# Kernel tuning notes

Measured on AMD Instinct MI355X. Metric: run time of the kernel, lower is better.

Reference implementation:

```python
import jax, jax.numpy as jnp
import numpy as np
import math

# dims matching init_kwargs
B, N, CS, CZ = 1, 512, 384, 128
H, C, PQ, PV = 8, 128, 8, 8
INF, EPS = 1e5, 1e-8

# ---- quaternion / motor helpers (PGA motor encoded as [qw,qx,qy,qz,tx,ty,tz,0]) ----

def quat_conj(q):
    return q * jnp.array([1.0, -1.0, -1.0, -1.0], q.dtype)

def quat_mul(a, b):
    aw, ax, ay, az = jnp.split(a, 4, -1)
    bw, bx, by, bz = jnp.split(b, 4, -1)
    return jnp.concatenate([
        aw*bw - ax*bx - ay*by - az*bz,
        aw*bx + ax*bw + ay*bz - az*by,
        aw*by - ax*bz + ay*bw + az*bx,
        aw*bz + ax*by - ay*bx + az*bw], -1)

def quat_rotate(q, v):
    qv = q[..., 1:]
    uv = jnp.cross(qv, v)
    uuv = jnp.cross(qv, uv)
    return v + 2.0 * (q[..., :1] * uv + uuv)

def point_trafo(p, q, t):
    # p [...,K,3]; rigid transform by frame motor, homogeneous 4-vector out
    pp = quat_rotate(q, p) + t
    return jnp.concatenate([pp, jnp.ones_like(pp[..., :1])], -1)

def mv_transform(mv, q, t):
    # versor sandwich on a 16-dim multivector: three rotatable 3-vector blocks,
    # the point block (7:10, weight at 10) also translates; slots 0 and 10:16 invariant
    s0 = mv[..., 0:1]
    v1 = quat_rotate(q, mv[..., 1:4])
    v2 = quat_rotate(q, mv[..., 4:7])
    w = mv[..., 10:11]
    p = quat_rotate(q, mv[..., 7:10]) + w * t
    return jnp.concatenate([s0, v1, v2, p, mv[..., 10:16]], -1)

def mv_transform_inv(mv, q, t):
    qc = quat_conj(q)
    s0 = mv[..., 0:1]
    v1 = quat_rotate(qc, mv[..., 1:4])
    v2 = quat_rotate(qc, mv[..., 4:7])
    w = mv[..., 10:11]
    p = quat_rotate(qc, mv[..., 7:10] - w * t)
    return jnp.concatenate([s0, v1, v2, p, mv[..., 10:16]], -1)


def _forward(s, g, z, T, mask, W_q, b_q, W_kv, b_kv, W_qp, b_qp, W_kp, b_kp,
             W_vg, b_vg, W_mg, W_b, b_b, W_dz, b_dz, head_weights,
             softmax_weights, W_out, b_out, W_geo):
    T8 = T[..., :8]                                      # extract_motor
    qn = T8[..., :4]
    qn = qn / jnp.sqrt(jnp.sum(qn**2, -1, keepdims=True) + EPS)
    tr = T8[..., 4:7]

    q = (s @ W_q + b_q).reshape(B, N, H, C)
    kv = (s @ W_kv + b_kv).reshape(B, N, H, 2 * C)
    k, v = kv[..., :C], kv[..., C:]

    def make_pts(W, bb):
        # split into 3 chunks + stack(dim=-1) == reshape(...,3,HP).swapaxes
        p = (s @ W + bb).reshape(B, N, 3, H * PQ).swapaxes(-1, -2)  # [B,N,HP,3]
        p4 = point_trafo(p, qn[:, :, None, :], tr[:, :, None, :])
        return p4.reshape(B, N, H, PQ, 4)

    q_pts = make_pts(W_qp, b_qp)
    k_pts = make_pts(W_kp, b_kp)

    v_g = (s @ W_vg + b_vg).reshape(B, N, PV, 16)
    v_g = jnp.einsum('oi,bnic->bnoc', W_mg,
                     jnp.concatenate([v_g, g], -2)).reshape(B, N, H, PV, 16)

    bias = jnp.einsum('bijz,zh->bhij', z, W_b) + b_b[None, :, None, None]
    a = jnp.einsum('bihc,bjhc->bhij', q, k) * math.sqrt(1.0 / (3 * C))
    a = a + math.sqrt(1.0 / 3.0) * bias

    disp = q_pts[:, :, None, :, :, :3] - k_pts[:, None, :, :, :, :3]  # [B,N,N,H,P,3]
    pt = jnp.sum(disp**2, -1)                                         # [B,N,N,H,P]
    hw = jax.nn.softplus(head_weights) * math.sqrt(1.0 / (3 * (PQ * 9.0 / 2)))
    pt = -0.5 * jnp.sum(pt * hw[None, None, None, :, None], -1)       # [B,N,N,H]

    sq_mask = INF * (mask[:, :, None] * mask[:, None, :] - 1.0)
    a = a + pt.transpose(0, 3, 1, 2) + sq_mask[:, None]
    a = jax.nn.softmax(softmax_weights[None, :, None, None] * a, axis=-1)

    o = jnp.einsum('bhij,bjhc->bihc', a, v)                           # [B,N,H,C]

    qb, tb = qn[:, :, None, None, :], tr[:, :, None, None, :]
    vg_glob = mv_transform(v_g, qb, tb)
    o_g = jnp.einsum('bhij,bjhpc->bihpc', a, vg_glob)
    o_g = mv_transform_inv(o_g, qb, tb)                               # [B,N,H,PV,16]
    n1 = jnp.sqrt(jnp.sum(o_g[..., :10]**2, -1) + EPS)
    n2 = jnp.sqrt(jnp.sum(o_g[..., 10:]**2, -1) + EPS)
    o_g_norm = jnp.stack([n1, n2], -1)                                # [B,N,H,PV,2]

    # local relative frame features (8 per head)
    q_rel = quat_mul(quat_conj(qn)[:, :, None, :], qn[:, None, :, :])
    t_rel = quat_rotate(quat_conj(qn)[:, :, None, :], tr[:, None, :, :] - tr[:, :, None, :])
    rel = jnp.concatenate([q_rel, t_rel, jnp.zeros_like(t_rel[..., :1])], -1)  # [B,N,N,8]
    o_rel = jnp.einsum('bhij,bijc->bihc', a, rel)

    o_pair = jnp.einsum('bhij,bijc->bihc', a, z @ W_dz + b_dz)        # [B,N,H,CZ//4]

    feats = jnp.concatenate([o_pair, o, o_rel,
                             o_g.reshape(B, N, H, PV * 16),
                             o_g_norm.reshape(B, N, H, PV * 2)], -1).reshape(B, N, -1)
    s_out = feats @ W_out + b_out                                     # [B,N,CS]
    g_out = jnp.einsum('oi,bnic->bnoc', W_geo, o_g.reshape(B, N, H * PV, 16))
    return s_out, g_out


def setup_inputs() -> dict:
    key = jax.random.key(0)
    ks = jax.random.split(key, 32)
    def rn(i, shape, sc=1.0):
        return sc * jax.random.normal(ks[i], shape, jnp.float32)
    s = rn(0, (B, N, CS))
    g = rn(1, (B, N, PV, 16))
    z = rn(2, (B, N, N, CZ))
    Traw = rn(3, (B, N, 16))
    qn = Traw[..., :4]
    qn = qn / jnp.sqrt(jnp.sum(qn**2, -1, keepdims=True) + 1e-8)
    T = Traw.at[..., :4].set(qn).at[..., 4:7].multiply(3.0).at[..., 7:].set(0.0)
    mask = jnp.ones((B, N), jnp.float32)
    w = 0.02
    CAT = H * (CZ // 4 + C + 8 + PV * 18)   # 2496
    return dict(
        s=s, g=g, z=z, T=T, mask=mask,
        W_q=rn(4, (CS, H * C), w), b_q=jnp.zeros((H * C,), jnp.float32),
        W_kv=rn(5, (CS, 2 * H * C), w), b_kv=jnp.zeros((2 * H * C,), jnp.float32),
        W_qp=rn(6, (CS, H * PQ * 3), w), b_qp=jnp.zeros((H * PQ * 3,), jnp.float32),
        W_kp=rn(7, (CS, H * PQ * 3), w), b_kp=jnp.zeros((H * PQ * 3,), jnp.float32),
        W_vg=rn(8, (CS, PV * 16), w), b_vg=jnp.zeros((PV * 16,), jnp.float32),
        W_mg=rn(9, (H * PV, 2 * PV), 0.1),
        W_b=rn(10, (CZ, H), w), b_b=jnp.zeros((H,), jnp.float32),
        W_dz=rn(11, (CZ, CZ // 4), w), b_dz=jnp.zeros((CZ // 4,), jnp.float32),
        head_weights=-2.0 + 0.3 * rn(12, (H,)),
        softmax_weights=jnp.ones((H,), jnp.float32) + 0.1 * rn(13, (H,)),
        W_out=rn(14, (CAT, CS), w), b_out=jnp.zeros((CS,), jnp.float32),
        W_geo=rn(15, (PV, H * PV), 0.1))


def reference(s, g, z, T, mask, W_q, b_q, W_kv, b_kv, W_qp, b_qp, W_kp, b_kp,
              W_vg, b_vg, W_mg, W_b, b_b, W_dz, b_dz, head_weights,
              softmax_weights, W_out, b_out, W_geo):
    return _forward(s, g, z, T, mask, W_q, b_q, W_kv, b_kv, W_qp, b_qp, W_kp,
                    b_kp, W_vg, b_vg, W_mg, W_b, b_b, W_dz, b_dz, head_weights,
                    softmax_weights, W_out, b_out, W_geo)
```

## Files before the change

### kernel.cpp

```cpp
#include <hip/hip_runtime.h>
#include <math.h>

#define NN 512
#define CSD 384
#define CZD 128
#define HD 8
#define CD 128
#define EPSV 1e-8f
#define INFV 100000.0f

#define OFF_QN    ((size_t)0)
#define OFF_TR    ((size_t)2048)
#define OFF_ROWT  ((size_t)4096)
#define OFF_COLT  ((size_t)8192)
#define OFF_SB    ((size_t)12288)
#define OFF_QBUF  ((size_t)45056)
#define OFF_KV    ((size_t)569344)
#define OFF_QPR   ((size_t)1617920)
#define OFF_KPR   ((size_t)1716224)
#define OFF_VGR   ((size_t)1814528)
#define OFF_ZB    ((size_t)1880064)
#define OFF_A     ((size_t)3977216)
#define OFF_U     ((size_t)6074368)
#define OFF_V     ((size_t)6729728)
#define OFF_VP    ((size_t)7385088)
#define OFF_OB0   ((size_t)8433664)
#define OFF_OB1   ((size_t)8957952)
#define OFF_OG0   ((size_t)9482240)
#define OFF_OG1   ((size_t)10006528)
#define OFF_FEATS ((size_t)10530816)
#define OFF_PS    ((size_t)11808768)

__device__ __forceinline__ void qrot(const float q[4], const float* v, float* out) {
    float qw = q[0], qx = q[1], qy = q[2], qz = q[3];
    float ux = qy*v[2] - qz*v[1];
    float uy = qz*v[0] - qx*v[2];
    float uz = qx*v[1] - qy*v[0];
    float uux = qy*uz - qz*uy;
    float uuy = qz*ux - qx*uz;
    float uuz = qx*uy - qy*ux;
    out[0] = v[0] + 2.0f*(qw*ux + uux);
    out[1] = v[1] + 2.0f*(qw*uy + uuy);
    out[2] = v[2] + 2.0f*(qw*uz + uuz);
}

__device__ __forceinline__ void gemm_tiles(const float* __restrict__ A, int lda,
                                           const float* __restrict__ B, int ldb,
                                           int m0, int n0, int k0, int nk,
                                           float acc[4][4], float* AsT, float* Bs) {
    int t = threadIdx.x;
    int tx = t & 15, ty = t >> 4;
    int arow = t >> 3, ak4 = (t & 7) << 2;
    int brow = t >> 4, bc4 = (t & 15) << 2;
    const float* Ap0 = A + (size_t)(m0 + arow)*lda + ak4;
    const float* Ap1 = A + (size_t)(m0 + arow + 32)*lda + ak4;
    const float* Bp0 = B + (size_t)brow*ldb + n0 + bc4;
    const float* Bp1 = B + (size_t)(brow + 16)*ldb + n0 + bc4;
    float4 a0 = *(const float4*)(Ap0 + k0);
    float4 a1 = *(const float4*)(Ap1 + k0);
    float4 b0 = *(const float4*)(Bp0 + (size_t)k0*ldb);
    float4 b1 = *(const float4*)(Bp1 + (size_t)k0*ldb);
    for (int kc = 0; kc < nk; kc++) {
        AsT[(ak4+0)*68 + arow] = a0.x;
        AsT[(ak4+1)*68 + arow] = a0.y;
        AsT[(ak4+2)*68 + arow] = a0.z;
        AsT[(ak4+3)*68 + arow] = a0.w;
        AsT[(ak4+0)*68 + arow+32] = a1.x;
        AsT[(ak4+1)*68 + arow+32] = a1.y;
        AsT[(ak4+2)*68 + arow+32] = a1.z;
        AsT[(ak4+3)*68 + arow+32] = a1.w;
        *(float4*)(Bs + brow*64 + bc4) = b0;
        *(float4*)(Bs + (brow+16)*64 + bc4) = b1;
        __syncthreads();
        if (kc + 1 < nk) {
            int kb = k0 + (kc+1)*32;
            a0 = *(const float4*)(Ap0 + kb);
            a1 = *(const float4*)(Ap1 + kb);
            b0 = *(const float4*)(Bp0 + (size_t)kb*ldb);
            b1 = *(const float4*)(Bp1 + (size_t)kb*ldb);
        }
        #pragma unroll
        for (int kk = 0; kk < 32; kk++) {
            float4 av = *(const float4*)(AsT + kk*68 + ty*4);
            float4 bv = *(const float4*)(Bs + kk*64 + tx*4);
            acc[0][0] += av.x*bv.x; acc[0][1] += av.x*bv.y; acc[0][2] += av.x*bv.z; acc[0][3] += av.x*bv.w;
            acc[1][0] += av.y*bv.x; acc[1][1] += av.y*bv.y; acc[1][2] += av.y*bv.z; acc[1][3] += av.y*bv.w;
            acc[2][0] += av.z*bv.x; acc[2][1] += av.z*bv.y; acc[2][2] += av.z*bv.z; acc[2][3] += av.z*bv.w;
            acc[3][0] += av.w*bv.x; acc[3][1] += av.w*bv.y; acc[3][2] += av.w*bv.z; acc[3][3] += av.w*bv.w;
        }
        __syncthreads();
    }
}


__global__ __launch_bounds__(256) void k_proj_all(const float* __restrict__ s,
    const float* __restrict__ W_q,  const float* __restrict__ b_q,  float* __restrict__ qbuf,
    const float* __restrict__ W_kv, const float* __restrict__ b_kv, float* __restrict__ kvb,
    const float* __restrict__ W_qp, const float* __restrict__ b_qp, float* __restrict__ qpr,
    const float* __restrict__ W_kp, const float* __restrict__ b_kp, float* __restrict__ kpr,
    const float* __restrict__ W_vg, const float* __restrict__ b_vg, float* __restrict__ vgr) {
    __shared__ float AsT[32*68];
    __shared__ float Bs[32*64];
    int ny = blockIdx.y;
    const float* W; const float* bias; float* C; int N; int n0;
    if (ny < 16)      { W=W_q;  bias=b_q;  C=qbuf; N=1024; n0=ny*64; }
    else if (ny < 48) { W=W_kv; bias=b_kv; C=kvb;  N=2048; n0=(ny-16)*64; }
    else if (ny < 51) { W=W_qp; bias=b_qp; C=qpr;  N=192;  n0=(ny-48)*64; }
    else if (ny < 54) { W=W_kp; bias=b_kp; C=kpr;  N=192;  n0=(ny-51)*64; }
    else              { W=W_vg; bias=b_vg; C=vgr;  N=128;  n0=(ny-54)*64; }
    int m0 = blockIdx.x*64;
    float acc[4][4] = {};
    gemm_tiles(s, CSD, W, N, m0, n0, 0, 12, acc, AsT, Bs);
    int tx = threadIdx.x & 15, ty = threadIdx.x >> 4;
    float4 bb = *(const float4*)(bias + n0 + tx*4);
    #pragma unroll
    for (int rr = 0; rr < 4; rr++) {
        float4 o = make_float4(acc[rr][0]+bb.x, acc[rr][1]+bb.y, acc[rr][2]+bb.z, acc[rr][3]+bb.w);
        *(float4*)(C + (size_t)(m0+ty*4+rr)*N + n0 + tx*4) = o;
    }
}

__global__ __launch_bounds__(256) void k_geo(
    const float* __restrict__ T,
    const float* __restrict__ qpr, const float* __restrict__ kpr,
    const float* __restrict__ vgr, const float* __restrict__ g,
    const float* __restrict__ W_mg,
    const float* __restrict__ qbuf, const float* __restrict__ kvb,
    const float* __restrict__ hwraw, const float* __restrict__ b_b,
    float* __restrict__ qn, float* __restrict__ tr,
    float* __restrict__ U, float* __restrict__ V,
    float* __restrict__ rowt, float* __restrict__ colt,
    float* __restrict__ Vp)
{
    __shared__ float s_q[4];
    __shared__ float s_t[3];
    __shared__ float s_qpts[192], s_kpts[192];
    __shared__ float s_Qsq[8], s_Ksq[8];
    int n = blockIdx.x, t = threadIdx.x;
    if (t == 0) {
        float q0=T[n*16+0], q1=T[n*16+1], q2=T[n*16+2], q3=T[n*16+3];
        float inv = 1.0f/sqrtf(q0*q0+q1*q1+q2*q2+q3*q3 + EPSV);
        float a0=q0*inv, a1=q1*inv, a2=q2*inv, a3=q3*inv;
        s_q[0]=a0; s_q[1]=a1; s_q[2]=a2; s_q[3]=a3;
        float u0=T[n*16+4], u1=T[n*16+5], u2=T[n*16+6];
        s_t[0]=u0; s_t[1]=u1; s_t[2]=u2;
        qn[n*4+0]=a0; qn[n*4+1]=a1; qn[n*4+2]=a2; qn[n*4+3]=a3;
        tr[n*3+0]=u0; tr[n*3+1]=u1; tr[n*3+2]=u2;
    }
    __syncthreads();
    float q[4]={s_q[0],s_q[1],s_q[2],s_q[3]};
    float t0=s_t[0], t1=s_t[1], t2=s_t[2];
    if (t < 128) {
        int m = t & 63;
        const float* raw = (t < 64) ? qpr : kpr;
        float p[3] = {raw[n*192 + m], raw[n*192 + 64 + m], raw[n*192 + 128 + m]};
        float r[3]; qrot(q,p,r);
        r[0]+=t0; r[1]+=t1; r[2]+=t2;
        float* dp = (t<64) ? s_qpts : s_kpts;
        dp[m*3+0]=r[0]; dp[m*3+1]=r[1]; dp[m*3+2]=r[2];
        float ss = r[0]*r[0]+r[1]*r[1]+r[2]*r[2];
        ss += __shfl_down(ss,4,8);
        ss += __shfl_down(ss,2,8);
        ss += __shfl_down(ss,1,8);
        if ((m&7)==0) ((t<64)?s_Qsq:s_Ksq)[m>>3] = ss;
    } else if (t < 192) {
        int o = t - 128;
        float in[16];
        #pragma unroll
        for (int c=0;c<16;c++){
            float acc=0.0f;
            #pragma unroll
            for (int i=0;i<8;i++)  acc += W_mg[o*16+i]*vgr[n*128+i*16+c];
            #pragma unroll
            for (int i=8;i<16;i++) acc += W_mg[o*16+i]*g[n*128+(i-8)*16+c];
            in[c]=acc;
        }
        float out[16];
        out[0]=in[0];
        qrot(q,in+1,out+1);
        qrot(q,in+4,out+4);
        float w=in[10];
        qrot(q,in+7,out+7);
        out[7]+=w*t0; out[8]+=w*t1; out[9]+=w*t2;
        #pragma unroll
        for (int c=10;c<16;c++) out[c]=in[c];
        int h=o>>3, pp=o&7;
        float* vp = Vp + ((size_t)(h*512+n))*256 + 128 + pp*16;
        #pragma unroll
        for (int c=0;c<16;c++) vp[c]=out[c];
    }
    #pragma unroll
    for (int l=0;l<4;l++){
        int f = t + l*256; int h = f>>7, c = f&127;
        Vp[((size_t)(h*512+n))*256 + c] = kvb[(size_t)n*2048 + h*256 + 128 + c];
    }
    __syncthreads();
    #pragma unroll
    for (int h = 0; h < 8; h++) {
        float hwv = log1pf(expf(hwraw[h])) * 0.09622504486493763f;
        if (t < 160) {
            float u, v;
            if (t < 128) {
                u = 0.05103103630798287f * qbuf[(size_t)n*1024 + h*128 + t];
                v = kvb[(size_t)n*2048 + h*256 + t];
            } else if (t < 152) {
                int d = t - 128;
                u = hwv * s_qpts[h*24 + d];
                v = s_kpts[h*24 + d];
            } else { u = 0.0f; v = 0.0f; }
            U[((size_t)h*512 + n)*160 + t] = u;
            V[((size_t)h*160 + t)*512 + n] = v;
        }
        if (t == 160) rowt[h*512+n] = -0.5f*hwv*s_Qsq[h] + 0.5773502691896258f*b_b[h] - INFV;
        if (t == 161) colt[h*512+n] = -0.5f*hwv*s_Ksq[h];
    }
}

__global__ __launch_bounds__(128) void k_zb(const float* __restrict__ z,
        const float* __restrict__ W_b, float* __restrict__ zb) {
    __shared__ float zt[64*132];
    __shared__ float part[8*64];
    int i = blockIdx.x, j0 = blockIdx.y*64;
    int t = threadIdx.x;
    #pragma unroll
    for (int l = 0; l < 16; l++) {
        int f = t + l*128;
        int row = f >> 5, c4 = (f & 31) << 2;
        float4 v = *(const float4*)(z + ((size_t)(i*NN) + j0 + row)*CZD + c4);
        *(float4*)(zt + row*132 + c4) = v;
    }
    __syncthreads();
    int w = t >> 6, j = t & 63;
    int cbase = w*64;
    float acc[8] = {};
    #pragma unroll
    for (int c16 = 0; c16 < 16; c16++) {
        float4 v = *(const float4*)(zt + j*132 + cbase + c16*4);
        int c = cbase + c16*4;
        #pragma unroll
        for (int h = 0; h < 8; h++)
            acc[h] += v.x*W_b[(c+0)*8+h] + v.y*W_b[(c+1)*8+h]
                    + v.z*W_b[(c+2)*8+h] + v.w*W_b[(c+3)*8+h];
    }
    if (w == 1) {
        #pragma unroll
        for (int h = 0; h < 8; h++) part[h*64 + j] = acc[h];
    }
    __syncthreads();
    if (w == 0) {
        #pragma unroll
        for (int h = 0; h < 8; h++)
            zb[((size_t)h*512 + i)*512 + j0 + j] = acc[h] + part[h*64 + j];
    }
}

__global__ __launch_bounds__(256) void k_scorefill(const float* __restrict__ U, const float* __restrict__ V,
        const float* __restrict__ rowt, const float* __restrict__ colt,
        const float* __restrict__ zb, const float* __restrict__ mask,
        const float* __restrict__ sw, float* __restrict__ Am) {
    __shared__ float AsT[32*68];
    __shared__ float Bs[32*64];
    int h = blockIdx.z;
    int m0 = blockIdx.x*64, n0 = blockIdx.y*64;
    float acc[4][4] = {};
    gemm_tiles(U + (size_t)h*512*160, 160, V + (size_t)h*160*512, 512, m0, n0, 0, 5, acc, AsT, Bs);
    int tx = threadIdx.x & 15, ty = threadIdx.x >> 4;
    float swh = sw[h];
    float4 ct = *(const float4*)(colt + h*512 + n0 + tx*4);
    float4 mj = *(const float4*)(mask + n0 + tx*4);
    #pragma unroll
    for (int rr = 0; rr < 4; rr++) {
        int i = m0 + ty*4 + rr;
        float rt = rowt[h*512 + i];
        float mi = mask[i] * INFV;
        float4 zv = *(const float4*)(zb + ((size_t)h*512 + i)*512 + n0 + tx*4);
        float4 r;
        r.x = (acc[rr][0] + rt + ct.x + 0.5773502691896258f*zv.x + mi*mj.x)*swh;
        r.y = (acc[rr][1] + rt + ct.y + 0.5773502691896258f*zv.y + mi*mj.y)*swh;
        r.z = (acc[rr][2] + rt + ct.z + 0.5773502691896258f*zv.z + mi*mj.z)*swh;
        r.w = (acc[rr][3] + rt + ct.w + 0.5773502691896258f*zv.w + mi*mj.w)*swh;
        *(float4*)(Am + ((size_t)h*512 + i)*512 + n0 + tx*4) = r;
    }
}

__global__ __launch_bounds__(256) void k_softmax(float* __restrict__ Am,
        const float* __restrict__ qn, const float* __restrict__ tr, float* __restrict__ S) {
    __shared__ float red[8];
    __shared__ float sred[4][8];
    int row = blockIdx.x;
    float* p = Am + (size_t)row*512;
    int t = threadIdx.x;
    float x0 = p[t], x1 = p[t+256];
    float m = fmaxf(x0, x1);
    #pragma unroll
    for (int o = 32; o > 0; o >>= 1) m = fmaxf(m, __shfl_xor(m, o));
    int wv = t >> 6, ln = t & 63;
    if (ln == 0) red[wv] = m;
    __syncthreads();
    m = fmaxf(fmaxf(red[0], red[1]), fmaxf(red[2], red[3]));
    float e0 = expf(x0 - m), e1 = expf(x1 - m);
    float sm = e0 + e1;
    #pragma unroll
    for (int o = 32; o > 0; o >>= 1) sm += __shfl_xor(sm, o);
    __syncthreads();
    if (ln == 0) red[4 + wv] = sm;
    __syncthreads();
    float inv = 1.0f / (red[4]+red[5]+red[6]+red[7]);
    float a0 = e0*inv, a1 = e1*inv;
    p[t] = a0;
    p[t+256] = a1;
    float4 q0 = *(const float4*)(qn + t*4);
    float4 q1 = *(const float4*)(qn + (t+256)*4);
    float acc[8];
    acc[0] = a0*q0.x + a1*q1.x;
    acc[1] = a0*q0.y + a1*q1.y;
    acc[2] = a0*q0.z + a1*q1.z;
    acc[3] = a0*q0.w + a1*q1.w;
    acc[4] = a0*tr[t*3+0] + a1*tr[(t+256)*3+0];
    acc[5] = a0*tr[t*3+1] + a1*tr[(t+256)*3+1];
    acc[6] = a0*tr[t*3+2] + a1*tr[(t+256)*3+2];
    acc[7] = a0 + a1;
    #pragma unroll
    for (int c = 0; c < 8; c++) {
        #pragma unroll
        for (int o = 32; o > 0; o >>= 1) acc[c] += __shfl_xor(acc[c], o);
    }
    if (ln == 0) {
        #pragma unroll
        for (int c = 0; c < 8; c++) sred[wv][c] = acc[c];
    }
    __syncthreads();
    if (t < 8) {
        int h = row >> 9, i = row & 511;
        S[i*64 + h*8 + t] = sred[0][t]+sred[1][t]+sred[2][t]+sred[3][t];
    }
}

__global__ __launch_bounds__(256) void k_apply(const float* __restrict__ Am,
        const float* __restrict__ Vp, float* __restrict__ ob0, float* __restrict__ ob1,
        float* __restrict__ og0, float* __restrict__ og1) {
    __shared__ float AsT[32*68];
    __shared__ float Bs[32*64];
    int m0 = blockIdx.x*64;
    int n0 = blockIdx.y*64;
    int h = blockIdx.z & 7, js = blockIdx.z >> 3;
    float acc[4][4] = {};
    gemm_tiles(Am + (size_t)h*512*512, 512, Vp + (size_t)h*512*256, 256,
               m0, n0, js*256, 8, acc, AsT, Bs);
    int tx = threadIdx.x & 15, ty = threadIdx.x >> 4;
    float* obuf = js ? ob1 : ob0;
    float* og   = js ? og1 : og0;
    float* base = (n0 < 128) ? (obuf + h*128 + n0) : (og + h*128 + n0 - 128);
    #pragma unroll
    for (int rr = 0; rr < 4; rr++) {
        *(float4*)(base + (size_t)(m0+ty*4+rr)*1024 + tx*4) =
            make_float4(acc[rr][0], acc[rr][1], acc[rr][2], acc[rr][3]);
    }
}

__global__ __launch_bounds__(256) void k_azfin(
    const float* __restrict__ Am, const float* __restrict__ z,
    const float* __restrict__ ob0, const float* __restrict__ ob1,
    const float* __restrict__ og0, const float* __restrict__ og1,
    const float* __restrict__ W_dz, const float* __restrict__ b_dz,
    const float* __restrict__ S, const float* __restrict__ qn, const float* __restrict__ tr,
    const float* __restrict__ W_geo,
    float* __restrict__ feats, float* __restrict__ outg)
{
    __shared__ float aT[512*8];
    __shared__ float part[3*1024];
    __shared__ float s_az[1024];
    __shared__ float s_og[1024];
    int i = blockIdx.x, t = threadIdx.x;
    #pragma unroll
    for (int l = 0; l < 16; l++) {
        int f = t + l*256;
        int h = f >> 9, j = f & 511;
        aT[j*8 + h] = Am[((size_t)h*512 + i)*512 + j];
    }
    __syncthreads();
    int c2 = t & 63, quarter = t >> 6;
    int jb = quarter*128;
    float acc[8][2] = {};
    for (int j = jb; j < jb+128; j++) {
        float2 zv = *(const float2*)(z + ((size_t)(i*NN) + j)*CZD + c2*2);
        float4 a0 = *(const float4*)(aT + j*8);
        float4 a1 = *(const float4*)(aT + j*8 + 4);
        acc[0][0] += a0.x*zv.x; acc[0][1] += a0.x*zv.y;
        acc[1][0] += a0.y*zv.x; acc[1][1] += a0.y*zv.y;
        acc[2][0] += a0.z*zv.x; acc[2][1] += a0.z*zv.y;
        acc[3][0] += a0.w*zv.x; acc[3][1] += a0.w*zv.y;
        acc[4][0] += a1.x*zv.x; acc[4][1] += a1.x*zv.y;
        acc[5][0] += a1.y*zv.x; acc[5][1] += a1.y*zv.y;
        acc[6][0] += a1.z*zv.x; acc[6][1] += a1.z*zv.y;
        acc[7][0] += a1.w*zv.x; acc[7][1] += a1.w*zv.y;
    }
    if (quarter > 0) {
        #pragma unroll
        for (int h = 0; h < 8; h++) {
            part[(quarter-1)*1024 + h*128 + c2*2 + 0] = acc[h][0];
            part[(quarter-1)*1024 + h*128 + c2*2 + 1] = acc[h][1];
        }
    }
    __syncthreads();
    if (quarter == 0) {
        #pragma unroll
        for (int h = 0; h < 8; h++) {
            #pragma unroll
            for (int d = 0; d < 2; d++) {
                s_az[h*128 + c2*2 + d] = acc[h][d] + part[h*128 + c2*2 + d]
                          + part[1024 + h*128 + c2*2 + d] + part[2048 + h*128 + c2*2 + d];
            }
        }
    }
    __syncthreads();
    float* f = feats + (size_t)i*2496;
    #pragma unroll
    for (int l = 0; l < 4; l++) {
        int ff = t + l*256; int h = ff>>7, c = ff&127;
        f[h*312 + 32 + c] = ob0[(size_t)i*1024 + h*128 + c] + ob1[(size_t)i*1024 + h*128 + c];
    }
    {
        int h = t >> 5, cdz = t & 31;
        float a2 = b_dz[cdz];
        #pragma unroll 4
        for (int zc = 0; zc < 128; zc++) a2 += s_az[h*128 + zc]*W_dz[zc*32 + cdz];
        f[h*312 + cdz] = a2;
    }
    float qc0=qn[i*4], qc1=-qn[i*4+1], qc2=-qn[i*4+2], qc3=-qn[i*4+3];
    float t0=tr[i*3], t1=tr[i*3+1], t2=tr[i*3+2];
    if (t < 64) {
        int h = t >> 3, p = t & 7;
        const float* a0 = og0 + (size_t)i*1024 + h*128 + p*16;
        const float* a1 = og1 + (size_t)i*1024 + h*128 + p*16;
        float in[16];
        #pragma unroll
        for (int c=0;c<16;c++) in[c]=a0[c]+a1[c];
        float qc[4]={qc0,qc1,qc2,qc3};
        float out[16];
        out[0]=in[0];
        qrot(qc,in+1,out+1);
        qrot(qc,in+4,out+4);
        float w=in[10];
        float tmp[3]={in[7]-w*t0, in[8]-w*t1, in[9]-w*t2};
        qrot(qc,tmp,out+7);
        #pragma unroll
        for (int c2x=10;c2x<16;c2x++) out[c2x]=in[c2x];
        float n1=EPSV, n2=EPSV;
        #pragma unroll
        for (int c2x=0;c2x<10;c2x++) n1 += out[c2x]*out[c2x];
        #pragma unroll
        for (int c2x=10;c2x<16;c2x++) n2 += out[c2x]*out[c2x];
        n1=sqrtf(n1); n2=sqrtf(n2);
        #pragma unroll
        for (int c2x=0;c2x<16;c2x++){ f[h*312+168+p*16+c2x]=out[c2x]; s_og[t*16+c2x]=out[c2x]; }
        f[h*312+296+p*2]=n1; f[h*312+296+p*2+1]=n2;
    } else if (t < 72) {
        int h = t - 64;
        const float* Sr = S + i*64 + h*8;
        float b0=Sr[0], b1=Sr[1], b2=Sr[2], b3=Sr[3];
        f[h*312+160] = qc0*b0 - qc1*b1 - qc2*b2 - qc3*b3;
        f[h*312+161] = qc0*b1 + qc1*b0 + qc2*b3 - qc3*b2;
        f[h*312+162] = qc0*b2 - qc1*b3 + qc2*b0 + qc3*b1;
        f[h*312+163] = qc0*b3 + qc1*b2 - qc2*b1 + qc3*b0;
        float A = Sr[7];
        float v[3]={Sr[4]-A*t0, Sr[5]-A*t1, Sr[6]-A*t2};
        float qc[4]={qc0,qc1,qc2,qc3};
        float r[3]; qrot(qc,v,r);
        f[h*312+164]=r[0]; f[h*312+165]=r[1]; f[h*312+166]=r[2]; f[h*312+167]=0.0f;
    }
    __syncthreads();
    if (t < 128) {
        int o = (t>>4) & 7, c = t & 15;
        float a3 = 0.0f;
        #pragma unroll 4
        for (int i2=0;i2<64;i2++) a3 += W_geo[o*64+i2]*s_og[i2*16+c];
        outg[(size_t)i*128 + o*16 + c] = a3;
    }
}

__global__ __launch_bounds__(256) void k_sout(const float* __restrict__ feats,
        const float* __restrict__ W_out, float* __restrict__ Ps) {
    __shared__ float AsT[32*68];
    __shared__ float Bs[32*64];
    int m0 = blockIdx.x*64, n0 = blockIdx.y*64, kz = blockIdx.z;
    float acc[4][4] = {};
    gemm_tiles(feats, 2496, W_out, CSD, m0, n0, kz*416, 13, acc, AsT, Bs);
    int tx = threadIdx.x & 15, ty = threadIdx.x >> 4;
    float* slab = Ps + (size_t)kz*512*384;
    #pragma unroll
    for (int rr = 0; rr < 4; rr++) {
        *(float4*)(slab + (size_t)(m0+ty*4+rr)*CSD + n0 + tx*4) =
            make_float4(acc[rr][0], acc[rr][1], acc[rr][2], acc[rr][3]);
    }
}

__global__ __launch_bounds__(256) void k_sout_red(const float* __restrict__ Ps,
        const float* __restrict__ b_out, float* __restrict__ out) {
    int idx = (blockIdx.x*256 + threadIdx.x)*4;
    float4 s = *(const float4*)(b_out + (idx % 384));
    #pragma unroll
    for (int kz = 0; kz < 6; kz++) {
        float4 p = *(const float4*)(Ps + (size_t)kz*196608 + idx);
        s.x += p.x; s.y += p.y; s.z += p.z; s.w += p.w;
    }
    *(float4*)(out + idx) = s;
}


extern "C" void kernel_launch(void* const* d_in, const int* in_sizes, int n_in,
                              void* d_out, int out_size, void* d_ws, size_t ws_size,
                              hipStream_t stream) {
    const float* s     = (const float*)d_in[0];
    const float* g     = (const float*)d_in[1];
    const float* z     = (const float*)d_in[2];
    const float* T     = (const float*)d_in[3];
    const float* mask  = (const float*)d_in[4];
    const float* W_q   = (const float*)d_in[5];
    const float* b_q   = (const float*)d_in[6];
    const float* W_kv  = (const float*)d_in[7];
    const float* b_kv  = (const float*)d_in[8];
    const float* W_qp  = (const float*)d_in[9];
    const float* b_qp  = (const float*)d_in[10];
    const float* W_kp  = (const float*)d_in[11];
    const float* b_kp  = (const float*)d_in[12];
    const float* W_vg  = (const float*)d_in[13];
    const float* b_vg  = (const float*)d_in[14];
    const float* W_mg  = (const float*)d_in[15];
    const float* W_b   = (const float*)d_in[16];
    const float* b_b   = (const float*)d_in[17];
    const float* W_dz  = (const float*)d_in[18];
    const float* b_dz  = (const float*)d_in[19];
    const float* hw    = (const float*)d_in[20];
    const float* sw    = (const float*)d_in[21];
    const float* W_out = (const float*)d_in[22];
    const float* b_out = (const float*)d_in[23];
    const float* W_geo = (const float*)d_in[24];

    float* ws   = (float*)d_ws;
    float* out  = (float*)d_out;

    float* qn   = ws + OFF_QN;
    float* tr   = ws + OFF_TR;
    float* rowt = ws + OFF_ROWT;
    float* colt = ws + OFF_COLT;
    float* Sbuf = ws + OFF_SB;
    float* qbuf = ws + OFF_QBUF;
    float* kvb  = ws + OFF_KV;
    float* qpr  = ws + OFF_QPR;
    float* kpr  = ws + OFF_KPR;
    float* vgr  = ws + OFF_VGR;
    float* zb   = ws + OFF_ZB;
    float* Am   = ws + OFF_A;
    float* U    = ws + OFF_U;
    float* V    = ws + OFF_V;
    float* Vp   = ws + OFF_VP;
    float* ob0  = ws + OFF_OB0;
    float* ob1  = ws + OFF_OB1;
    float* og0  = ws + OFF_OG0;
    float* og1  = ws + OFF_OG1;
    float* feats= ws + OFF_FEATS;
    float* Ps   = ws + OFF_PS;

    k_proj_all<<<dim3(8,56),256,0,stream>>>(s, W_q,b_q,qbuf, W_kv,b_kv,kvb,
                                            W_qp,b_qp,qpr, W_kp,b_kp,kpr, W_vg,b_vg,vgr);
    k_geo<<<NN,256,0,stream>>>(T,qpr,kpr,vgr,g,W_mg,qbuf,kvb,hw,b_b,
                               qn,tr,U,V,rowt,colt,Vp);
    k_zb<<<dim3(NN,8),128,0,stream>>>(z,W_b,zb);
    k_scorefill<<<dim3(8,8,8),256,0,stream>>>(U,V,rowt,colt,zb,mask,sw,Am);
    k_softmax<<<4096,256,0,stream>>>(Am,qn,tr,Sbuf);
    k_apply<<<dim3(8,4,16),256,0,stream>>>(Am,Vp,ob0,ob1,og0,og1);
    k_azfin<<<NN,256,0,stream>>>(Am,z,ob0,ob1,og0,og1,W_dz,b_dz,Sbuf,qn,tr,W_geo,
                                 feats, out + (size_t)NN*CSD);
    k_sout<<<dim3(8,6,6),256,0,stream>>>(feats,W_out,Ps);
    k_sout_red<<<192,256,0,stream>>>(Ps,b_out,out);
}
```

Before: 405.1 us.

## Use split-bf16 MFMA for score and apply GEMMs

Replaces the FP32 SIMT tiled GEMM in the score and attention-apply kernels with MFMA 16x16x32 bf16 instructions. Each fp32 operand is split into high and low bf16 parts, and three MFMA products are accumulated to keep close to fp32 accuracy. The V matrix layout changes to row-major [h][n][160] so it can be loaded like A. The new epilogues write scalar, strided outputs instead of float4, and the bf16 conversion adds ALU and LDS work.

```diff
diff --git a/kernel.cpp b/kernel.cpp
--- a/kernel.cpp
+++ b/kernel.cpp
@@ -31,6 +31,10 @@
 #define OFF_FEATS ((size_t)10530816)
 #define OFF_PS    ((size_t)11808768)
 
+typedef __attribute__((ext_vector_type(4))) float f32x4;
+typedef __attribute__((ext_vector_type(8))) short bf16x8;
+typedef __attribute__((ext_vector_type(4))) short s16x4;
+
 __device__ __forceinline__ void qrot(const float q[4], const float* v, float* out) {
     float qw = q[0], qx = q[1], qy = q[2], qz = q[3];
     float ux = qy*v[2] - qz*v[1];
@@ -42,6 +46,87 @@
     out[0] = v[0] + 2.0f*(qw*ux + uux);
     out[1] = v[1] + 2.0f*(qw*uy + uuy);
     out[2] = v[2] + 2.0f*(qw*uz + uuz);
+}
+
+__device__ __forceinline__ void cvt2(float x, unsigned short& h, unsigned short& lo) {
+    unsigned u = __float_as_uint(x);
+    unsigned r = (u + 0x7FFFu + ((u >> 16) & 1u)) >> 16;
+    h = (unsigned short)r;
+    float hf = __uint_as_float(r << 16);
+    float lf = x - hf;
+    unsigned u2 = __float_as_uint(lf);
+    unsigned r2 = (u2 + 0x7FFFu + ((u2 >> 16) & 1u)) >> 16;
+    lo = (unsigned short)r2;
+}
+
+__device__ __forceinline__ void stA(short* H, short* L, int row, int k4, float4 v) {
+    unsigned short h0,l0,h1,l1,h2,l2,h3,l3;
+    cvt2(v.x,h0,l0); cvt2(v.y,h1,l1); cvt2(v.z,h2,l2); cvt2(v.w,h3,l3);
+    s16x4 vh = {(short)h0,(short)h1,(short)h2,(short)h3};
+    s16x4 vl = {(short)l0,(short)l1,(short)l2,(short)l3};
+    *(s16x4*)(H + row*40 + k4) = vh;
+    *(s16x4*)(L + row*40 + k4) = vl;
+}
+__device__ __forceinline__ void stBT(short* H, short* L, int k, int n4, float4 v) {
+    unsigned short h, lo;
+    cvt2(v.x,h,lo); H[(n4+0)*40+k]=(short)h; L[(n4+0)*40+k]=(short)lo;
+    cvt2(v.y,h,lo); H[(n4+1)*40+k]=(short)h; L[(n4+1)*40+k]=(short)lo;
+    cvt2(v.z,h,lo); H[(n4+2)*40+k]=(short)h; L[(n4+2)*40+k]=(short)lo;
+    cvt2(v.w,h,lo); H[(n4+3)*40+k]=(short)h; L[(n4+3)*40+k]=(short)lo;
+}
+
+template<int BT>
+__device__ __forceinline__ void mfma_tiles(const float* __restrict__ A, int lda,
+                                           const float* __restrict__ B, int ldb,
+                                           int m0, int n0, int k0, int nk,
+                                           f32x4* acc,
+                                           short* Ah, short* Al, short* Bh, short* Bl) {
+    int t = threadIdx.x;
+    int w = t >> 6, l = t & 63, g = l >> 4, li = l & 15;
+    int ar = t >> 3, ak = (t & 7) << 2;
+    const float* Ap0 = A + (size_t)(m0 + ar)*lda + ak;
+    const float* Ap1 = A + (size_t)(m0 + ar + 32)*lda + ak;
+    const float* Bp0; const float* Bp1;
+    int bk = t >> 4, bn = (t & 15) << 2;
+    if (BT) {
+        Bp0 = B + (size_t)(n0 + ar)*ldb + ak;
+        Bp1 = B + (size_t)(n0 + ar + 32)*ldb + ak;
+    } else {
+        Bp0 = B + (size_t)bk*ldb + n0 + bn;
+        Bp1 = B + (size_t)(bk + 16)*ldb + n0 + bn;
+    }
+    float4 a0 = *(const float4*)(Ap0 + k0);
+    float4 a1 = *(const float4*)(Ap1 + k0);
+    float4 b0, b1;
+    if (BT) { b0 = *(const float4*)(Bp0 + k0); b1 = *(const float4*)(Bp1 + k0); }
+    else    { b0 = *(const float4*)(Bp0 + (size_t)k0*ldb); b1 = *(const float4*)(Bp1 + (size_t)k0*ldb); }
+    for (int kc = 0; kc < nk; kc++) {
+        stA(Ah, Al, ar, ak, a0);
+        stA(Ah, Al, ar+32, ak, a1);
+        if (BT) { stA(Bh, Bl, ar, ak, b0); stA(Bh, Bl, ar+32, ak, b1); }
+        else    { stBT(Bh, Bl, bk, bn, b0); stBT(Bh, Bl, bk+16, bn, b1); }
+        __syncthreads();
+        if (kc + 1 < nk) {
+            int kb = k0 + (kc+1)*32;
+            a0 = *(const float4*)(Ap0 + kb);
+            a1 = *(const float4*)(Ap1 + kb);
+            if (BT) { b0 = *(const float4*)(Bp0 + kb); b1 = *(const float4*)(Bp1 + kb); }
+            else { b0 = *(const float4*)(Bp0 + (size_t)kb*ldb); b1 = *(const float4*)(Bp1 + (size_t)kb*ldb); }
+        }
+        int arow = (w*16 + li)*40 + g*8;
+        bf16x8 avh = *(bf16x8*)(Ah + arow);
+        bf16x8 avl = *(bf16x8*)(Al + arow);
+        #pragma unroll
+        for (int c = 0; c < 4; c++) {
+            int brow = (c*16 + li)*40 + g*8;
+            bf16x8 bvh = *(bf16x8*)(Bh + brow);
+            bf16x8 bvl = *(bf16x8*)(Bl + brow);
+            acc[c] = __builtin_amdgcn_mfma_f32_16x16x32_bf16(avh, bvh, acc[c], 0, 0, 0);
+            acc[c] = __builtin_amdgcn_mfma_f32_16x16x32_bf16(avh, bvl, acc[c], 0, 0, 0);
+            acc[c] = __builtin_amdgcn_mfma_f32_16x16x32_bf16(avl, bvh, acc[c], 0, 0, 0);
+        }
+        __syncthreads();
+    }
 }
 
 __device__ __forceinline__ void gemm_tiles(const float* __restrict__ A, int lda,
@@ -209,7 +294,7 @@
                 v = s_kpts[h*24 + d];
             } else { u = 0.0f; v = 0.0f; }
             U[((size_t)h*512 + n)*160 + t] = u;
-            V[((size_t)h*160 + t)*512 + n] = v;
+            V[((size_t)h*512 + n)*160 + t] = v;
         }
         if (t == 160) rowt[h*512+n] = -0.5f*hwv*s_Qsq[h] + 0.5773502691896258f*b_b[h] - INFV;
         if (t == 161) colt[h*512+n] = -0.5f*hwv*s_Ksq[h];
@@ -258,28 +343,28 @@
         const float* __restrict__ rowt, const float* __restrict__ colt,
         const float* __restrict__ zb, const float* __restrict__ mask,
         const float* __restrict__ sw, float* __restrict__ Am) {
-    __shared__ float AsT[32*68];
-    __shared__ float Bs[32*64];
+    __shared__ short Ah[64*40], Al[64*40], Bh[64*40], Bl[64*40];
     int h = blockIdx.z;
     int m0 = blockIdx.x*64, n0 = blockIdx.y*64;
-    float acc[4][4] = {};
-    gemm_tiles(U + (size_t)h*512*160, 160, V + (size_t)h*160*512, 512, m0, n0, 0, 5, acc, AsT, Bs);
-    int tx = threadIdx.x & 15, ty = threadIdx.x >> 4;
+    f32x4 acc[4] = {};
+    mfma_tiles<1>(U + (size_t)h*512*160, 160, V + (size_t)h*512*160, 160,
+                  m0, n0, 0, 5, acc, Ah, Al, Bh, Bl);
+    int t = threadIdx.x, w = t >> 6, l = t & 63, g = l >> 4, li = l & 15;
     float swh = sw[h];
-    float4 ct = *(const float4*)(colt + h*512 + n0 + tx*4);
-    float4 mj = *(const float4*)(mask + n0 + tx*4);
-    #pragma unroll
-    for (int rr = 0; rr < 4; rr++) {
-        int i = m0 + ty*4 + rr;
-        float rt = rowt[h*512 + i];
-        float mi = mask[i] * INFV;
-        float4 zv = *(const float4*)(zb + ((size_t)h*512 + i)*512 + n0 + tx*4);
-        float4 r;
-        r.x = (acc[rr][0] + rt + ct.x + 0.5773502691896258f*zv.x + mi*mj.x)*swh;
-        r.y = (acc[rr][1] + rt + ct.y + 0.5773502691896258f*zv.y + mi*mj.y)*swh;
-        r.z = (acc[rr][2] + rt + ct.z + 0.5773502691896258f*zv.z + mi*mj.z)*swh;
-        r.w = (acc[rr][3] + rt + ct.w + 0.5773502691896258f*zv.w + mi*mj.w)*swh;
-        *(float4*)(Am + ((size_t)h*512 + i)*512 + n0 + tx*4) = r;
+    #pragma unroll
+    for (int c = 0; c < 4; c++) {
+        int j = n0 + c*16 + li;
+        float ct = colt[h*512 + j];
+        float mj = mask[j];
+        #pragma unroll
+        for (int r = 0; r < 4; r++) {
+            int i = m0 + w*16 + g*4 + r;
+            float rt = rowt[h*512 + i];
+            float mi = mask[i]*INFV;
+            float zv = zb[((size_t)h*512 + i)*512 + j];
+            Am[((size_t)h*512 + i)*512 + j] =
+                (acc[c][r] + rt + ct + 0.5773502691896258f*zv + mi*mj)*swh;
+        }
     }
 }
 
@@ -339,22 +424,25 @@
 __global__ __launch_bounds__(256) void k_apply(const float* __restrict__ Am,
         const float* __restrict__ Vp, float* __restrict__ ob0, float* __restrict__ ob1,
         float* __restrict__ og0, float* __restrict__ og1) {
-    __shared__ float AsT[32*68];
-    __shared__ float Bs[32*64];
+    __shared__ short Ah[64*40], Al[64*40], Bh[64*40], Bl[64*40];
     int m0 = blockIdx.x*64;
     int n0 = blockIdx.y*64;
     int h = blockIdx.z & 7, js = blockIdx.z >> 3;
-    float acc[4][4] = {};
-    gemm_tiles(Am + (size_t)h*512*512, 512, Vp + (size_t)h*512*256, 256,
-               m0, n0, js*256, 8, acc, AsT, Bs);
-    int tx = threadIdx.x & 15, ty = threadIdx.x >> 4;
+    f32x4 acc[4] = {};
+    mfma_tiles<0>(Am + (size_t)h*512*512, 512, Vp + (size_t)h*512*256, 256,
+                  m0, n0, js*256, 8, acc, Ah, Al, Bh, Bl);
+    int t = threadIdx.x, w = t >> 6, l = t & 63, g = l >> 4, li = l & 15;
     float* obuf = js ? ob1 : ob0;
     float* og   = js ? og1 : og0;
-    float* base = (n0 < 128) ? (obuf + h*128 + n0) : (og + h*128 + n0 - 128);
-    #pragma unroll
-    for (int rr = 0; rr < 4; rr++) {
-        *(float4*)(base + (size_t)(m0+ty*4+rr)*1024 + tx*4) =
-            make_float4(acc[rr][0], acc[rr][1], acc[rr][2], acc[rr][3]);
+    #pragma unroll
+    for (int c = 0; c < 4; c++) {
+        int col = n0 + c*16 + li;
+        float* base = (col < 128) ? (obuf + h*128 + col) : (og + h*128 + col - 128);
+        #pragma unroll
+        for (int r = 0; r < 4; r++) {
+            int i = m0 + w*16 + g*4 + r;
+            base[(size_t)i*1024] = acc[c][r];
+        }
     }
 }
 
```

New measurement: 402.1 us. Within noise of the previous version (-0.7%).
